# Kernel tuning notes

Hardware: AMD Instinct MI355X
Metric: run time of the kernel (lower is better)

Reference implementation:

```python
import jax, jax.numpy as jnp
import numpy as np

B, L, C = 4, 2052, 1024
H, D = 16, 64          # num_heads, head_dim
NREG = 4               # register tokens, bypass RoPE
LN_EPS = 1e-5


def setup_inputs() -> dict:
    key = jax.random.key(0)
    ks = jax.random.split(key, 6)
    s = 1.0 / np.sqrt(C)
    return {
        "x": jax.random.normal(ks[0], (B, L, C), jnp.float32),
        "rope_embed": jax.random.normal(ks[1], (2, L - NREG, D), jnp.float32),  # [cos; sin]
        "Wqkv": jax.random.normal(ks[2], (C, 3 * C), jnp.float32) * s,
        "bqkv": jnp.zeros((3 * C,), jnp.float32),
        "Wproj": jax.random.normal(ks[3], (C, C), jnp.float32) * s,
        "bproj": jnp.zeros((C,), jnp.float32),
        "ln_gamma": jnp.ones((C,), jnp.float32),
        "ln_beta": jnp.zeros((C,), jnp.float32),
    }


def _rotate_half(x):
    x1, x2 = jnp.split(x, 2, axis=-1)
    return jnp.concatenate([-x2, x1], axis=-1)


def _apply_rope(q, k, rope_embed, n_reg):
    # q,k: (B,H,L,D); rope_embed: (2, L-n_reg, D)
    cos = rope_embed[0][None, None]  # (1,1,Ls,D)
    sin = rope_embed[1][None, None]
    def rot(t):
        reg, sp = t[:, :, :n_reg], t[:, :, n_reg:]
        sp = sp * cos + _rotate_half(sp) * sin
        return jnp.concatenate([reg, sp], axis=2)
    return rot(q), rot(k)


def reference(x, rope_embed, Wqkv, bqkv, Wproj, bproj, ln_gamma, ln_beta):
    # QKV projection: (B,L,3C) -> (3,B,H,L,D)
    qkv = (x @ Wqkv + bqkv).reshape(B, L, 3, H, D).transpose(2, 0, 3, 1, 4)
    q, k, v = qkv[0], qkv[1], qkv[2]
    q, k = _apply_rope(q, k, rope_embed, NREG)
    # SDPA (no dropout, not causal)
    scale = 1.0 / np.sqrt(D)
    logits = jnp.einsum("bhqd,bhkd->bhqk", q, k) * scale
    attn = jax.nn.softmax(logits, axis=-1)
    out = jnp.einsum("bhqk,bhkd->bhqd", attn, v)
    out = out.transpose(0, 2, 1, 3).reshape(B, L, C)
    # post-attention LayerNorm
    mu = jnp.mean(out, axis=-1, keepdims=True)
    var = jnp.mean(jnp.square(out - mu), axis=-1, keepdims=True)
    out = (out - mu) * jax.lax.rsqrt(var + LN_EPS) * ln_gamma + ln_beta
    # output projection
    return out @ Wproj + bproj
```

## Files before the change

kernel.cpp:

```cpp
#include <hip/hip_runtime.h>
#include <hip/hip_bf16.h>

#define B_ 4
#define L_ 2052
#define C_ 1024
#define H_ 16
#define D_ 64
#define NREG_ 4
#define M_ (B_*L_)
#define LP_ 2056
#define QSC 0.18033688f

typedef short bf16x8 __attribute__((ext_vector_type(8)));
typedef float f32x4 __attribute__((ext_vector_type(4)));
typedef __hip_bfloat16 bf16;

#define MFMA(a,b,c) __builtin_amdgcn_mfma_f32_16x16x32_bf16(a,b,c,0,0,0)

__device__ inline float b2f(bf16 v){ return __bfloat162float(v); }
__device__ inline bf16  f2b(float v){ return __float2bfloat16(v); }
__device__ inline bf16x8 as8(int4 v){ union{int4 i; bf16x8 b;} u; u.i=v; return u.b; }

__device__ inline void gl_lds16(const void* g, void* l){
    __builtin_amdgcn_global_load_lds(
        (const __attribute__((address_space(1))) void*)g,
        (__attribute__((address_space(3))) void*)l,
        16, 0, 0);
}

__global__ __launch_bounds__(256)
void cvt_split(const float* __restrict__ in, bf16* __restrict__ hi,
               bf16* __restrict__ lo, int n)
{
    int i = (blockIdx.x*256 + threadIdx.x)*4;
    if (i >= n) return;
    float4 v = *(const float4*)(in + i);
    int2 hraw, lraw;
    bf16* hp = (bf16*)&hraw;
    bf16* lp = (bf16*)&lraw;
    float vv[4] = {v.x, v.y, v.z, v.w};
    #pragma unroll
    for (int j=0;j<4;++j){
        bf16 h = f2b(vv[j]);
        hp[j] = h;
        lp[j] = f2b(vv[j] - b2f(h));
    }
    *(int2*)(hi + i) = hraw;
    *(int2*)(lo + i) = lraw;
}

__global__ __launch_bounds__(256)
void transpose_cvt(const float* __restrict__ in, bf16* __restrict__ out,
                   int R, int Cc)
{
    __shared__ bf16 t[32][33];
    int bx = blockIdx.x * 32;
    int by = blockIdx.y * 32;
    int tx = threadIdx.x;
    int ty = threadIdx.y;
    #pragma unroll
    for (int i=0;i<4;++i){
        int r = by + ty + i*8;
        int c = bx + tx;
        t[ty+i*8][tx] = f2b(in[(size_t)r*Cc + c]);
    }
    __syncthreads();
    #pragma unroll
    for (int i=0;i<4;++i){
        int r = bx + ty + i*8;
        int c = by + tx;
        out[(size_t)r*R + c] = t[tx][ty+i*8];
    }
}

template<typename OutT, bool SPLIT>
__global__ __launch_bounds__(256,2)
void gemm_wide(const bf16* __restrict__ A, const bf16* __restrict__ Alo,
               const bf16* __restrict__ Bt, const float* __restrict__ bias,
               OutT* __restrict__ C, int M, int N, int K)
{
    __shared__ bf16 As[128*32];
    __shared__ bf16 Als[SPLIT ? 128*32 : 8];
    __shared__ bf16 Bs[256*32];

    int tid  = threadIdx.x;
    int lane = tid & 63, wave = tid >> 6;
    int wm = (wave>>1)*64, wn = (wave&1)*128;
    int bm = blockIdx.y*128, bn = blockIdx.x*256;
    int lrow = lane & 15;
    int quad = lane >> 4;
    int sw8  = (quad ^ ((lrow>>2)&3)) * 8;

    f32x4 acc[4][8] = {};

    for (int k0 = 0; k0 < K; k0 += 32) {
        #pragma unroll
        for (int it=0; it<2; ++it) {
            int o  = (wave*2+it)*1024 + lane*16;
            int r  = o >> 6;
            int p  = (o >> 4) & 3;
            int ls = p ^ ((r>>2)&3);
            int ga = bm + r; if (ga >= M) ga = M-1;
            gl_lds16(A + (size_t)ga*K + k0 + ls*8, &As[(wave*2+it)*512]);
            if constexpr (SPLIT)
                gl_lds16(Alo + (size_t)ga*K + k0 + ls*8, &Als[(wave*2+it)*512]);
        }
        #pragma unroll
        for (int it=0; it<4; ++it) {
            int o  = (wave*4+it)*1024 + lane*16;
            int r  = o >> 6;
            int p  = (o >> 4) & 3;
            int ls = p ^ ((r>>2)&3);
            gl_lds16(Bt + (size_t)(bn + r)*K + k0 + ls*8, &Bs[(wave*4+it)*512]);
        }
        __syncthreads();

        bf16x8 b[8];
        #pragma unroll
        for (int i=0;i<8;++i)
            b[i] = *(const bf16x8*)(&Bs[(wn+i*16+lrow)*32 + sw8]);
        #pragma unroll
        for (int mi=0;mi<4;++mi){
            bf16x8 a = *(const bf16x8*)(&As[(wm+mi*16+lrow)*32 + sw8]);
            #pragma unroll
            for (int ni=0;ni<8;++ni)
                acc[mi][ni] = MFMA(a, b[ni], acc[mi][ni]);
            if constexpr (SPLIT) {
                bf16x8 al = *(const bf16x8*)(&Als[(wm+mi*16+lrow)*32 + sw8]);
                #pragma unroll
                for (int ni=0;ni<8;++ni)
                    acc[mi][ni] = MFMA(al, b[ni], acc[mi][ni]);
            }
        }
        __syncthreads();
    }

    #pragma unroll
    for (int ni=0;ni<8;++ni){
        int col = bn + wn + ni*16 + lrow;
        float bv = bias[col];
        #pragma unroll
        for (int mi=0;mi<4;++mi){
            int rowb = bm + wm + mi*16 + quad*4;
            #pragma unroll
            for (int r=0;r<4;++r){
                int row = rowb + r;
                if (row < M) {
                    float v = acc[mi][ni][r] + bv;
                    if constexpr (sizeof(OutT)==4) C[(size_t)row*N + col] = v;
                    else                           C[(size_t)row*N + col] = f2b(v);
                }
            }
        }
    }
}

__global__ __launch_bounds__(256)
void rope_kernel(bf16* __restrict__ qkv, const float* __restrict__ rope)
{
    int idx = blockIdx.x*256 + threadIdx.x;
    int d = idx & 31;
    int h = (idx >> 5) & 15;
    int m = idx >> 9;
    if (m >= M_) return;
    int l = m % L_;
    if (l < NREG_) return;
    const float* cp = rope + (size_t)(l - NREG_)*D_;
    const float* sp = rope + (size_t)(L_ - NREG_)*D_ + (size_t)(l - NREG_)*D_;
    float c0 = cp[d], c1 = cp[d+32], s0 = sp[d], s1 = sp[d+32];
    size_t base = (size_t)m*3072 + h*64;
    {
        float a = b2f(qkv[base + d]), b = b2f(qkv[base + d + 32]);
        qkv[base + d]      = f2b(a*c0 - b*s0);
        qkv[base + d + 32] = f2b(b*c1 + a*s1);
    }
    {
        size_t kb = base + 1024;
        float a = b2f(qkv[kb + d]), b = b2f(qkv[kb + d + 32]);
        qkv[kb + d]      = f2b(a*c0 - b*s0);
        qkv[kb + d + 32] = f2b(b*c1 + a*s1);
    }
}

__global__ __launch_bounds__(256)
void transpose_v(const bf16* __restrict__ qkv, bf16* __restrict__ Vt)
{
    __shared__ bf16 t[64*72];
    int bh = blockIdx.y, lt = blockIdx.x;
    int b = bh >> 4, h = bh & 15;
    int tid = threadIdx.x;
    #pragma unroll
    for (int it=0; it<2; ++it){
        int i = tid + it*256;
        int il = i >> 3, c = (i&7)*8;
        int l = lt*64 + il;
        int4 v = {0,0,0,0};
        if (l < L_) v = *(const int4*)(qkv + ((size_t)b*L_ + l)*3072 + 2048 + h*64 + c);
        *(int4*)(&t[il*72 + c]) = v;
    }
    __syncthreads();
    #pragma unroll
    for (int it=0; it<2; ++it){
        int i = tid + it*256;
        int d = i >> 3, ck = (i&7)*8;
        if (lt*64 + ck + 8 <= LP_){
            union { int4 q; bf16 e[8]; } u;
            #pragma unroll
            for (int j=0;j<8;++j) u.e[j] = t[(ck+j)*72 + d];
            *(int4*)(&Vt[((size_t)bh*64 + d)*LP_ + lt*64 + ck]) = u.q;
        }
    }
}

__global__ __launch_bounds__(256)
void attn_kernel(const bf16* __restrict__ qkv, const bf16* __restrict__ Vt,
                 float* __restrict__ out)
{
    __shared__ bf16 sQ[128*72];
    __shared__ bf16 sK[64*72];
    __shared__ bf16 sV[64*72];

    int tid = threadIdx.x, lane = tid & 63, wave = tid >> 6;
    int lrow = lane & 15, lk8 = (lane>>4)*8, quad = lane >> 4;
    int qt = blockIdx.x, bh = blockIdx.y;
    int b  = bh >> 4, h = bh & 15;
    size_t rowbase = (size_t)b * L_;
    int q0 = qt * 128;

    #pragma unroll
    for (int it=0; it<4; ++it){
        int i = tid + it*256;
        int r = i >> 3;
        int c = (i & 7) * 8;
        int lq = q0 + r;
        int4 v = {0,0,0,0};
        if (lq < L_) v = *(const int4*)(qkv + (rowbase + lq)*3072 + h*64 + c);
        *(int4*)(&sQ[r*72 + c]) = v;
    }
    __syncthreads();

    bf16x8 qf[2][2];
    #pragma unroll
    for (int qi=0;qi<2;++qi)
        #pragma unroll
        for (int s=0;s<2;++s)
            qf[qi][s] = *(const bf16x8*)(&sQ[(wave*32 + qi*16 + lrow)*72 + s*32 + lk8]);

    f32x4 o_[2][4] = {};
    f32x4 lsum[2] = {};

    bf16x8 onesf;
    #pragma unroll
    for (int j=0;j<8;++j) onesf[j] = (short)0x3F80;

    const int nkt = (L_ + 63) / 64;

    int4 kr[2], vr[2];
    {
        #pragma unroll
        for (int it=0; it<2; ++it){
            int i = tid + it*256;
            int r = i >> 3, c = (i & 7)*8;
            int pr = (r & 0x23) | ((r & 0x0C) << 1) | ((r & 0x10) >> 2);
            kr[it] = *(const int4*)(qkv + (rowbase + pr)*3072 + 1024 + h*64 + c);
            vr[it] = *(const int4*)(Vt + ((size_t)bh*64 + r)*LP_ + c);
        }
    }

    for (int kt = 0; kt < nkt; ++kt) {
        __syncthreads();
        #pragma unroll
        for (int it=0; it<2; ++it){
            int i = tid + it*256;
            int r = i >> 3, c = (i & 7)*8;
            *(int4*)(&sK[r*72 + c]) = kr[it];
            *(int4*)(&sV[r*72 + c]) = vr[it];
        }
        __syncthreads();
        if (kt+1 < nkt){
            #pragma unroll
            for (int it=0; it<2; ++it){
                int i = tid + it*256;
                int r = i >> 3, c = (i & 7)*8;
                int pr = (r & 0x23) | ((r & 0x0C) << 1) | ((r & 0x10) >> 2);
                int lk = (kt+1)*64 + pr;
                kr[it] = (lk < L_) ? *(const int4*)(qkv + (rowbase+lk)*3072 + 1024 + h*64 + c)
                                   : (int4){0,0,0,0};
                int vc = (kt+1)*64 + c;
                vr[it] = (vc + 8 <= LP_) ? *(const int4*)(Vt + ((size_t)bh*64 + r)*LP_ + vc)
                                         : (int4){0,0,0,0};
            }
        }

        bool full = (kt != 32);
        int4 pb[2][2];

        #pragma unroll
        for (int ki=0; ki<4; ++ki){
            bf16x8 kf0 = *(const bf16x8*)(&sK[(ki*16+lrow)*72 + lk8]);
            bf16x8 kf1 = *(const bf16x8*)(&sK[(ki*16+lrow)*72 + 32 + lk8]);
            #pragma unroll
            for (int qi=0; qi<2; ++qi){
                f32x4 t = {};
                t = MFMA(kf0, qf[qi][0], t);
                t = MFMA(kf1, qf[qi][1], t);
                float p[4];
                #pragma unroll
                for (int r=0;r<4;++r){
                    float e = __builtin_amdgcn_exp2f(t[r]*QSC);
                    int keyi = (ki>>1)*32 + quad*8 + (ki&1)*4 + r;
                    p[r] = (full || (2048 + keyi) < L_) ? e : 0.f;
                }
                union { int2 d2; __hip_bfloat162 h2[2]; } u;
                u.h2[0] = __float22bfloat162_rn({p[0], p[1]});
                u.h2[1] = __float22bfloat162_rn({p[2], p[3]});
                if ((ki & 1) == 0){ pb[qi][ki>>1].x = u.d2.x; pb[qi][ki>>1].y = u.d2.y; }
                else              { pb[qi][ki>>1].z = u.d2.x; pb[qi][ki>>1].w = u.d2.y; }
            }
        }

        #pragma unroll
        for (int ni=0; ni<4; ++ni){
            bf16x8 vf0 = *(const bf16x8*)(&sV[(ni*16+lrow)*72 + lk8]);
            bf16x8 vf1 = *(const bf16x8*)(&sV[(ni*16+lrow)*72 + 32 + lk8]);
            #pragma unroll
            for (int mi=0; mi<2; ++mi){
                f32x4 t = o_[mi][ni];
                t = MFMA(vf0, as8(pb[mi][0]), t);
                t = MFMA(vf1, as8(pb[mi][1]), t);
                o_[mi][ni] = t;
            }
        }
        #pragma unroll
        for (int mi=0; mi<2; ++mi){
            lsum[mi] = MFMA(onesf, as8(pb[mi][0]), lsum[mi]);
            lsum[mi] = MFMA(onesf, as8(pb[mi][1]), lsum[mi]);
        }
    }

    #pragma unroll
    for (int mi=0; mi<2; ++mi){
        float inv = 1.f / lsum[mi][0];
        int lq = q0 + wave*32 + mi*16 + lrow;
        if (lq < L_){
            size_t base = (rowbase + lq)*1024 + h*64;
            #pragma unroll
            for (int ni=0; ni<4; ++ni){
                f32x4 t = o_[mi][ni];
                float4 w = {t[0]*inv, t[1]*inv, t[2]*inv, t[3]*inv};
                *(float4*)(&out[base + ni*16 + quad*4]) = w;
            }
        }
    }
}

__global__ __launch_bounds__(256)
void ln_kernel(const float* __restrict__ in, const float* __restrict__ gamma,
               const float* __restrict__ beta, bf16* __restrict__ y)
{
    int row = blockIdx.x;
    int tid = threadIdx.x;
    int wave = tid >> 6, lane = tid & 63;
    float4 v4 = *(const float4*)(in + (size_t)row*1024 + tid*4);
    float v[4] = {v4.x, v4.y, v4.z, v4.w};
    float s = 0.f, q = 0.f;
    #pragma unroll
    for (int j=0;j<4;++j){ s += v[j]; q += v[j]*v[j]; }
    #pragma unroll
    for (int o=1;o<64;o<<=1){ s += __shfl_xor(s, o); q += __shfl_xor(q, o); }
    __shared__ float sh[8];
    if (lane == 0){ sh[wave] = s; sh[4+wave] = q; }
    __syncthreads();
    s = sh[0]+sh[1]+sh[2]+sh[3];
    q = sh[4]+sh[5]+sh[6]+sh[7];
    float mu  = s * (1.f/1024.f);
    float var = q * (1.f/1024.f) - mu*mu;
    float rstd = rsqrtf(var + 1e-5f);
    int2 raw;
    bf16* ob = (bf16*)&raw;
    #pragma unroll
    for (int j=0;j<4;++j){
        float g = gamma[tid*4+j], be = beta[tid*4+j];
        ob[j] = f2b((v[j]-mu)*rstd*g + be);
    }
    *(int2*)(y + (size_t)row*1024 + tid*4) = raw;
}

extern "C" void kernel_launch(void* const* d_in, const int* in_sizes, int n_in,
                              void* d_out, int out_size, void* d_ws, size_t ws_size,
                              hipStream_t stream)
{
    const float* x     = (const float*)d_in[0];
    const float* rope  = (const float*)d_in[1];
    const float* Wqkv  = (const float*)d_in[2];
    const float* bqkv  = (const float*)d_in[3];
    const float* Wproj = (const float*)d_in[4];
    const float* bproj = (const float*)d_in[5];
    const float* lng   = (const float*)d_in[6];
    const float* lnb   = (const float*)d_in[7];
    float* out = (float*)d_out;

    char* ws = (char*)d_ws;
    size_t off = 0;
    auto alloc = [&](size_t bytes)->char* {
        char* p = ws + off;
        off += (bytes + 255) & ~(size_t)255;
        return p;
    };
    bf16* xhi    = (bf16*)alloc((size_t)M_*C_*2);
    bf16* xlo    = (bf16*)alloc((size_t)M_*C_*2);
    bf16* WqkvT  = (bf16*)alloc((size_t)3*C_*C_*2);
    bf16* WprojT = (bf16*)alloc((size_t)C_*C_*2);
    bf16* qkv    = (bf16*)alloc((size_t)M_*3*C_*2);
    bf16* Vt     = (bf16*)alloc((size_t)B_*H_*D_*LP_*2);

    float* attnF = (float*)xhi;
    bf16*  y     = qkv;

    cvt_split<<<M_*C_/1024, 256, 0, stream>>>(x, xhi, xlo, M_*C_);
    transpose_cvt<<<dim3(3*C_/32, C_/32), dim3(32,8), 0, stream>>>(Wqkv, WqkvT, C_, 3*C_);
    transpose_cvt<<<dim3(C_/32, C_/32), dim3(32,8), 0, stream>>>(Wproj, WprojT, C_, C_);
    gemm_wide<bf16, true><<<dim3(3*C_/256, (M_+127)/128), 256, 0, stream>>>(
        xhi, xlo, WqkvT, bqkv, qkv, M_, 3*C_, C_);
    rope_kernel<<<(M_*H_*32)/256, 256, 0, stream>>>(qkv, rope);
    transpose_v<<<dim3((L_+63)/64, B_*H_), 256, 0, stream>>>(qkv, Vt);
    attn_kernel<<<dim3((L_+127)/128, B_*H_), 256, 0, stream>>>(qkv, Vt, attnF);
    ln_kernel<<<M_, 256, 0, stream>>>(attnF, lng, lnb, y);
    gemm_wide<float, false><<<dim3(C_/256, (M_+127)/128), 256, 0, stream>>>(
        y, nullptr, WprojT, bproj, out, M_, C_, C_);
}
```

Before: 434.6 us.

## Double-buffer GEMM LDS tiles and fold hi/lo split into K dimension

The GEMM now keeps two LDS buffers and issues the global-to-LDS loads for the next K tile while the current tile is computed, so memory latency can overlap with MFMA work. The hi/lo bf16 split of x is stored side by side as one 2048-wide A matrix, and the B matrix index wraps at KB, so the split becomes a longer K loop instead of a second inner MFMA pass. LDS use per block doubles, which may lower occupancy. The code relies on a single barrier per iteration to order the async LDS loads against the reads.

```diff
diff --git a/kernel.cpp b/kernel.cpp
--- a/kernel.cpp
+++ b/kernel.cpp
@@ -29,8 +29,7 @@
 }
 
 __global__ __launch_bounds__(256)
-void cvt_split(const float* __restrict__ in, bf16* __restrict__ hi,
-               bf16* __restrict__ lo, int n)
+void cvt_split(const float* __restrict__ in, bf16* __restrict__ a2, int n)
 {
     int i = (blockIdx.x*256 + threadIdx.x)*4;
     if (i >= n) return;
@@ -45,8 +44,10 @@
         hp[j] = h;
         lp[j] = f2b(vv[j] - b2f(h));
     }
-    *(int2*)(hi + i) = hraw;
-    *(int2*)(lo + i) = lraw;
+    int row = i >> 10, col = i & 1023;
+    size_t base = (size_t)row*2048 + col;
+    *(int2*)(a2 + base)        = hraw;
+    *(int2*)(a2 + base + 1024) = lraw;
 }
 
 __global__ __launch_bounds__(256)
@@ -73,15 +74,14 @@
     }
 }
 
-template<typename OutT, bool SPLIT>
+template<typename OutT>
 __global__ __launch_bounds__(256,2)
-void gemm_wide(const bf16* __restrict__ A, const bf16* __restrict__ Alo,
-               const bf16* __restrict__ Bt, const float* __restrict__ bias,
-               OutT* __restrict__ C, int M, int N, int K)
-{
-    __shared__ bf16 As[128*32];
-    __shared__ bf16 Als[SPLIT ? 128*32 : 8];
-    __shared__ bf16 Bs[256*32];
+void gemm_dbuf(const bf16* __restrict__ A, const bf16* __restrict__ Bt,
+               const float* __restrict__ bias, OutT* __restrict__ C,
+               int M, int N, int K, int KB)
+{
+    __shared__ bf16 As[2][128*32];
+    __shared__ bf16 Bs[2][256*32];
 
     int tid  = threadIdx.x;
     int lane = tid & 63, wave = tid >> 6;
@@ -93,7 +93,8 @@
 
     f32x4 acc[4][8] = {};
 
-    for (int k0 = 0; k0 < K; k0 += 32) {
+    auto STAGE = [&](int buf, int k0){
+        int kb = (k0 >= KB) ? k0 - KB : k0;
         #pragma unroll
         for (int it=0; it<2; ++it) {
             int o  = (wave*2+it)*1024 + lane*16;
@@ -101,9 +102,7 @@
             int p  = (o >> 4) & 3;
             int ls = p ^ ((r>>2)&3);
             int ga = bm + r; if (ga >= M) ga = M-1;
-            gl_lds16(A + (size_t)ga*K + k0 + ls*8, &As[(wave*2+it)*512]);
-            if constexpr (SPLIT)
-                gl_lds16(Alo + (size_t)ga*K + k0 + ls*8, &Als[(wave*2+it)*512]);
+            gl_lds16(A + (size_t)ga*K + k0 + ls*8, &As[buf][(wave*2+it)*512]);
         }
         #pragma unroll
         for (int it=0; it<4; ++it) {
@@ -111,28 +110,31 @@
             int r  = o >> 6;
             int p  = (o >> 4) & 3;
             int ls = p ^ ((r>>2)&3);
-            gl_lds16(Bt + (size_t)(bn + r)*K + k0 + ls*8, &Bs[(wave*4+it)*512]);
-        }
-        __syncthreads();
+            gl_lds16(Bt + (size_t)(bn + r)*KB + kb + ls*8, &Bs[buf][(wave*4+it)*512]);
+        }
+    };
+
+    int nt = K >> 5;
+    int cur = 0;
+    STAGE(0, 0);
+    __syncthreads();
+
+    for (int t = 0; t < nt; ++t) {
+        if (t+1 < nt) STAGE(cur^1, (t+1)*32);
 
         bf16x8 b[8];
         #pragma unroll
         for (int i=0;i<8;++i)
-            b[i] = *(const bf16x8*)(&Bs[(wn+i*16+lrow)*32 + sw8]);
+            b[i] = *(const bf16x8*)(&Bs[cur][(wn+i*16+lrow)*32 + sw8]);
         #pragma unroll
         for (int mi=0;mi<4;++mi){
-            bf16x8 a = *(const bf16x8*)(&As[(wm+mi*16+lrow)*32 + sw8]);
+            bf16x8 a = *(const bf16x8*)(&As[cur][(wm+mi*16+lrow)*32 + sw8]);
             #pragma unroll
             for (int ni=0;ni<8;++ni)
                 acc[mi][ni] = MFMA(a, b[ni], acc[mi][ni]);
-            if constexpr (SPLIT) {
-                bf16x8 al = *(const bf16x8*)(&Als[(wm+mi*16+lrow)*32 + sw8]);
-                #pragma unroll
-                for (int ni=0;ni<8;++ni)
-                    acc[mi][ni] = MFMA(al, b[ni], acc[mi][ni]);
-            }
         }
         __syncthreads();
+        cur ^= 1;
     }
 
     #pragma unroll
@@ -407,25 +409,24 @@
         off += (bytes + 255) & ~(size_t)255;
         return p;
     };
-    bf16* xhi    = (bf16*)alloc((size_t)M_*C_*2);
-    bf16* xlo    = (bf16*)alloc((size_t)M_*C_*2);
+    bf16* A2     = (bf16*)alloc((size_t)M_*2048*2);
     bf16* WqkvT  = (bf16*)alloc((size_t)3*C_*C_*2);
     bf16* WprojT = (bf16*)alloc((size_t)C_*C_*2);
     bf16* qkv    = (bf16*)alloc((size_t)M_*3*C_*2);
     bf16* Vt     = (bf16*)alloc((size_t)B_*H_*D_*LP_*2);
 
-    float* attnF = (float*)xhi;
+    float* attnF = (float*)A2;
     bf16*  y     = qkv;
 
-    cvt_split<<<M_*C_/1024, 256, 0, stream>>>(x, xhi, xlo, M_*C_);
+    cvt_split<<<M_*C_/1024, 256, 0, stream>>>(x, A2, M_*C_);
     transpose_cvt<<<dim3(3*C_/32, C_/32), dim3(32,8), 0, stream>>>(Wqkv, WqkvT, C_, 3*C_);
     transpose_cvt<<<dim3(C_/32, C_/32), dim3(32,8), 0, stream>>>(Wproj, WprojT, C_, C_);
-    gemm_wide<bf16, true><<<dim3(3*C_/256, (M_+127)/128), 256, 0, stream>>>(
-        xhi, xlo, WqkvT, bqkv, qkv, M_, 3*C_, C_);
+    gemm_dbuf<bf16><<<dim3(3*C_/256, (M_+127)/128), 256, 0, stream>>>(
+        A2, WqkvT, bqkv, qkv, M_, 3*C_, 2048, C_);
     rope_kernel<<<(M_*H_*32)/256, 256, 0, stream>>>(qkv, rope);
     transpose_v<<<dim3((L_+63)/64, B_*H_), 256, 0, stream>>>(qkv, Vt);
     attn_kernel<<<dim3((L_+127)/128, B_*H_), 256, 0, stream>>>(qkv, Vt, attnF);
     ln_kernel<<<M_, 256, 0, stream>>>(attnF, lng, lnb, y);
-    gemm_wide<float, false><<<dim3(C_/256, (M_+127)/128), 256, 0, stream>>>(
-        y, nullptr, WprojT, bproj, out, M_, C_, C_);
-}
+    gemm_dbuf<float><<<dim3(C_/256, (M_+127)/128), 256, 0, stream>>>(
+        y, WprojT, bproj, out, M_, C_, C_, C_);
+}
```

New measurement: 475.0 us. +9.3%, slower.

## Load K/V MFMA fragments directly from global memory, dropping LDS staging

Applied to the files above, without the earlier changes.

The attention kernel no longer stages K and V tiles through shared memory with register prefetch and two barriers per tile. Each lane instead loads its MFMA fragments straight from global (L2-cached) memory, and the final partial key tile is peeled out of the loop so the masking check leaves the main loop. This removes the LDS round-trip and the per-tile synchronisation. In exchange, every wave re-reads K/V from global memory, with more redundant traffic and latency exposed, since there is no explicit prefetch.

```diff
diff --git a/kernel.cpp b/kernel.cpp
--- a/kernel.cpp
+++ b/kernel.cpp
@@ -217,8 +217,6 @@
                  float* __restrict__ out)
 {
     __shared__ bf16 sQ[128*72];
-    __shared__ bf16 sK[64*72];
-    __shared__ bf16 sV[64*72];
 
     int tid = threadIdx.x, lane = tid & 63, wave = tid >> 6;
     int lrow = lane & 15, lk8 = (lane>>4)*8, quad = lane >> 4;
@@ -253,52 +251,73 @@
     #pragma unroll
     for (int j=0;j<8;++j) onesf[j] = (short)0x3F80;
 
-    const int nkt = (L_ + 63) / 64;
-
-    int4 kr[2], vr[2];
+    int pk[4];
+    #pragma unroll
+    for (int ki=0;ki<4;++ki){
+        int s = ki*16 + lrow;
+        pk[ki] = (s & 0x23) | ((s & 0x0C) << 1) | ((s & 0x10) >> 2);
+    }
+
+    const bf16* kbase = qkv + rowbase*3072 + 1024 + h*64 + lk8;
+    const bf16* vbase = Vt + (size_t)bh*64*LP_ + lk8;
+
+    for (int kt = 0; kt < 32; ++kt) {
+        int4 pb[2][2];
+
+        const bf16* kb = kbase + (size_t)kt*64*3072;
+        #pragma unroll
+        for (int ki=0; ki<4; ++ki){
+            const bf16* kp = kb + (size_t)pk[ki]*3072;
+            bf16x8 kf0 = *(const bf16x8*)(kp);
+            bf16x8 kf1 = *(const bf16x8*)(kp + 32);
+            #pragma unroll
+            for (int qi=0; qi<2; ++qi){
+                f32x4 t = {};
+                t = MFMA(kf0, qf[qi][0], t);
+                t = MFMA(kf1, qf[qi][1], t);
+                float p[4];
+                #pragma unroll
+                for (int r=0;r<4;++r)
+                    p[r] = __builtin_amdgcn_exp2f(t[r]*QSC);
+                union { int2 d2; __hip_bfloat162 h2[2]; } u;
+                u.h2[0] = __float22bfloat162_rn({p[0], p[1]});
+                u.h2[1] = __float22bfloat162_rn({p[2], p[3]});
+                if ((ki & 1) == 0){ pb[qi][ki>>1].x = u.d2.x; pb[qi][ki>>1].y = u.d2.y; }
+                else              { pb[qi][ki>>1].z = u.d2.x; pb[qi][ki>>1].w = u.d2.y; }
+            }
+        }
+
+        const bf16* vb = vbase + kt*64;
+        #pragma unroll
+        for (int ni=0; ni<4; ++ni){
+            const bf16* vp = vb + (size_t)(ni*16+lrow)*LP_;
+            bf16x8 vf0 = *(const bf16x8*)(vp);
+            bf16x8 vf1 = *(const bf16x8*)(vp + 32);
+            #pragma unroll
+            for (int mi=0; mi<2; ++mi){
+                f32x4 t = o_[mi][ni];
+                t = MFMA(vf0, as8(pb[mi][0]), t);
+                t = MFMA(vf1, as8(pb[mi][1]), t);
+                o_[mi][ni] = t;
+            }
+        }
+        #pragma unroll
+        for (int mi=0; mi<2; ++mi){
+            lsum[mi] = MFMA(onesf, as8(pb[mi][0]), lsum[mi]);
+            lsum[mi] = MFMA(onesf, as8(pb[mi][1]), lsum[mi]);
+        }
+    }
+
     {
-        #pragma unroll
-        for (int it=0; it<2; ++it){
-            int i = tid + it*256;
-            int r = i >> 3, c = (i & 7)*8;
-            int pr = (r & 0x23) | ((r & 0x0C) << 1) | ((r & 0x10) >> 2);
-            kr[it] = *(const int4*)(qkv + (rowbase + pr)*3072 + 1024 + h*64 + c);
-            vr[it] = *(const int4*)(Vt + ((size_t)bh*64 + r)*LP_ + c);
-        }
-    }
-
-    for (int kt = 0; kt < nkt; ++kt) {
-        __syncthreads();
-        #pragma unroll
-        for (int it=0; it<2; ++it){
-            int i = tid + it*256;
-            int r = i >> 3, c = (i & 7)*8;
-            *(int4*)(&sK[r*72 + c]) = kr[it];
-            *(int4*)(&sV[r*72 + c]) = vr[it];
-        }
-        __syncthreads();
-        if (kt+1 < nkt){
-            #pragma unroll
-            for (int it=0; it<2; ++it){
-                int i = tid + it*256;
-                int r = i >> 3, c = (i & 7)*8;
-                int pr = (r & 0x23) | ((r & 0x0C) << 1) | ((r & 0x10) >> 2);
-                int lk = (kt+1)*64 + pr;
-                kr[it] = (lk < L_) ? *(const int4*)(qkv + (rowbase+lk)*3072 + 1024 + h*64 + c)
-                                   : (int4){0,0,0,0};
-                int vc = (kt+1)*64 + c;
-                vr[it] = (vc + 8 <= LP_) ? *(const int4*)(Vt + ((size_t)bh*64 + r)*LP_ + vc)
-                                         : (int4){0,0,0,0};
-            }
-        }
-
-        bool full = (kt != 32);
         int4 pb[2][2];
-
+        const bf16* kb = kbase + (size_t)2048*3072;
         #pragma unroll
         for (int ki=0; ki<4; ++ki){
-            bf16x8 kf0 = *(const bf16x8*)(&sK[(ki*16+lrow)*72 + lk8]);
-            bf16x8 kf1 = *(const bf16x8*)(&sK[(ki*16+lrow)*72 + 32 + lk8]);
+            int row = 2048 + pk[ki];
+            const bf16* kp = (row < L_) ? (kb + (size_t)pk[ki]*3072)
+                                        : (kbase);
+            bf16x8 kf0 = *(const bf16x8*)(kp);
+            bf16x8 kf1 = *(const bf16x8*)(kp + 32);
             #pragma unroll
             for (int qi=0; qi<2; ++qi){
                 f32x4 t = {};
@@ -309,7 +328,7 @@
                 for (int r=0;r<4;++r){
                     float e = __builtin_amdgcn_exp2f(t[r]*QSC);
                     int keyi = (ki>>1)*32 + quad*8 + (ki&1)*4 + r;
-                    p[r] = (full || (2048 + keyi) < L_) ? e : 0.f;
+                    p[r] = (2048 + keyi < L_) ? e : 0.f;
                 }
                 union { int2 d2; __hip_bfloat162 h2[2]; } u;
                 u.h2[0] = __float22bfloat162_rn({p[0], p[1]});
@@ -319,10 +338,13 @@
             }
         }
 
+        const bf16* vb = vbase + 2048;
         #pragma unroll
         for (int ni=0; ni<4; ++ni){
-            bf16x8 vf0 = *(const bf16x8*)(&sV[(ni*16+lrow)*72 + lk8]);
-            bf16x8 vf1 = *(const bf16x8*)(&sV[(ni*16+lrow)*72 + 32 + lk8]);
+            bf16x8 vf0 = {};
+            bf16x8 vf1 = {};
+            if (lk8 == 0)
+                vf0 = *(const bf16x8*)(vb + (size_t)(ni*16+lrow)*LP_);
             #pragma unroll
             for (int mi=0; mi<2; ++mi){
                 f32x4 t = o_[mi][ni];
```

After: 583.6 us. 34.3% more time.

## Load attention tiles via direct global-to-LDS with XOR swizzle, larger Q tile

Applied to the files above, without the earlier changes.

The attention kernel now stages Q, K and V tiles with global_load_lds directly into shared memory using an XOR-swizzled 64-wide layout instead of padded 72-wide rows. This drops the register-staged prefetch. Each block now covers 192 query rows (48 per wave), up from 128, to reuse K/V more, and launch bounds request 2 blocks per CU. The cost is that loads are no longer overlapped with compute (load, sync, compute, sync), register pressure rises from the bigger accumulators, and the grid shrinks.

```diff
diff --git a/kernel.cpp b/kernel.cpp
--- a/kernel.cpp
+++ b/kernel.cpp
@@ -212,95 +212,83 @@
     }
 }
 
-__global__ __launch_bounds__(256)
+__global__ __launch_bounds__(256,2)
 void attn_kernel(const bf16* __restrict__ qkv, const bf16* __restrict__ Vt,
                  float* __restrict__ out)
 {
-    __shared__ bf16 sQ[128*72];
-    __shared__ bf16 sK[64*72];
-    __shared__ bf16 sV[64*72];
+    __shared__ bf16 sQ[192*64];
+    __shared__ bf16 sK[64*64];
+    __shared__ bf16 sV[64*64];
 
     int tid = threadIdx.x, lane = tid & 63, wave = tid >> 6;
-    int lrow = lane & 15, lk8 = (lane>>4)*8, quad = lane >> 4;
+    int lrow = lane & 15, quad = lane >> 4;
     int qt = blockIdx.x, bh = blockIdx.y;
     int b  = bh >> 4, h = bh & 15;
     size_t rowbase = (size_t)b * L_;
-    int q0 = qt * 128;
-
-    #pragma unroll
-    for (int it=0; it<4; ++it){
-        int i = tid + it*256;
-        int r = i >> 3;
-        int c = (i & 7) * 8;
-        int lq = q0 + r;
-        int4 v = {0,0,0,0};
-        if (lq < L_) v = *(const int4*)(qkv + (rowbase + lq)*3072 + h*64 + c);
-        *(int4*)(&sQ[r*72 + c]) = v;
+    int q0 = qt * 192;
+
+    int l8   = lane >> 3;
+    int p3   = lane & 7;
+    int swz0 = (quad     ^ (lrow&7))*8;
+    int swz1 = ((4+quad) ^ (lrow&7))*8;
+
+    #pragma unroll
+    for (int it=0; it<6; ++it){
+        int ci  = wave*6 + it;
+        int row = ci*8 + l8;
+        int ls  = p3 ^ (row&7);
+        int gq  = q0 + row; if (gq >= L_) gq = L_-1;
+        gl_lds16(qkv + (rowbase + gq)*3072 + h*64 + ls*8, &sQ[ci*512]);
     }
     __syncthreads();
 
-    bf16x8 qf[2][2];
-    #pragma unroll
-    for (int qi=0;qi<2;++qi)
-        #pragma unroll
-        for (int s=0;s<2;++s)
-            qf[qi][s] = *(const bf16x8*)(&sQ[(wave*32 + qi*16 + lrow)*72 + s*32 + lk8]);
-
-    f32x4 o_[2][4] = {};
-    f32x4 lsum[2] = {};
+    bf16x8 qf[3][2];
+    #pragma unroll
+    for (int qi=0;qi<3;++qi){
+        qf[qi][0] = *(const bf16x8*)(&sQ[(wave*48 + qi*16 + lrow)*64 + swz0]);
+        qf[qi][1] = *(const bf16x8*)(&sQ[(wave*48 + qi*16 + lrow)*64 + swz1]);
+    }
+
+    f32x4 o_[3][4] = {};
+    f32x4 lsum[3] = {};
 
     bf16x8 onesf;
     #pragma unroll
     for (int j=0;j<8;++j) onesf[j] = (short)0x3F80;
 
-    const int nkt = (L_ + 63) / 64;
-
-    int4 kr[2], vr[2];
-    {
+    const bf16* kgbase = qkv + rowbase*3072 + 1024 + h*64;
+    const bf16* vgbase = Vt + (size_t)bh*64*LP_;
+
+    for (int kt = 0; kt <= 32; ++kt) {
         #pragma unroll
         for (int it=0; it<2; ++it){
-            int i = tid + it*256;
-            int r = i >> 3, c = (i & 7)*8;
-            int pr = (r & 0x23) | ((r & 0x0C) << 1) | ((r & 0x10) >> 2);
-            kr[it] = *(const int4*)(qkv + (rowbase + pr)*3072 + 1024 + h*64 + c);
-            vr[it] = *(const int4*)(Vt + ((size_t)bh*64 + r)*LP_ + c);
-        }
-    }
-
-    for (int kt = 0; kt < nkt; ++kt) {
+            int ci  = wave*2 + it;
+            int row = ci*8 + l8;
+            int ls  = p3 ^ (row&7);
+            int key = kt*64 + ((row & 0x23) | ((row & 0x0C) << 1) | ((row & 0x10) >> 2));
+            if (key >= L_) key = L_-1;
+            gl_lds16(kgbase + (size_t)key*3072 + ls*8, &sK[ci*512]);
+        }
+        #pragma unroll
+        for (int it=0; it<2; ++it){
+            int ci  = wave*2 + it;
+            int row = ci*8 + l8;
+            int ls  = p3 ^ (row&7);
+            int col = kt*64 + ls*8;
+            if (col + 8 > LP_) col = 0;
+            gl_lds16(vgbase + (size_t)row*LP_ + col, &sV[ci*512]);
+        }
         __syncthreads();
-        #pragma unroll
-        for (int it=0; it<2; ++it){
-            int i = tid + it*256;
-            int r = i >> 3, c = (i & 7)*8;
-            *(int4*)(&sK[r*72 + c]) = kr[it];
-            *(int4*)(&sV[r*72 + c]) = vr[it];
-        }
-        __syncthreads();
-        if (kt+1 < nkt){
-            #pragma unroll
-            for (int it=0; it<2; ++it){
-                int i = tid + it*256;
-                int r = i >> 3, c = (i & 7)*8;
-                int pr = (r & 0x23) | ((r & 0x0C) << 1) | ((r & 0x10) >> 2);
-                int lk = (kt+1)*64 + pr;
-                kr[it] = (lk < L_) ? *(const int4*)(qkv + (rowbase+lk)*3072 + 1024 + h*64 + c)
-                                   : (int4){0,0,0,0};
-                int vc = (kt+1)*64 + c;
-                vr[it] = (vc + 8 <= LP_) ? *(const int4*)(Vt + ((size_t)bh*64 + r)*LP_ + vc)
-                                         : (int4){0,0,0,0};
-            }
-        }
 
         bool full = (kt != 32);
-        int4 pb[2][2];
+        int4 pb[3][2];
 
         #pragma unroll
         for (int ki=0; ki<4; ++ki){
-            bf16x8 kf0 = *(const bf16x8*)(&sK[(ki*16+lrow)*72 + lk8]);
-            bf16x8 kf1 = *(const bf16x8*)(&sK[(ki*16+lrow)*72 + 32 + lk8]);
-            #pragma unroll
-            for (int qi=0; qi<2; ++qi){
+            bf16x8 kf0 = *(const bf16x8*)(&sK[(ki*16+lrow)*64 + swz0]);
+            bf16x8 kf1 = *(const bf16x8*)(&sK[(ki*16+lrow)*64 + swz1]);
+            #pragma unroll
+            for (int qi=0; qi<3; ++qi){
                 f32x4 t = {};
                 t = MFMA(kf0, qf[qi][0], t);
                 t = MFMA(kf1, qf[qi][1], t);
@@ -321,10 +309,10 @@
 
         #pragma unroll
         for (int ni=0; ni<4; ++ni){
-            bf16x8 vf0 = *(const bf16x8*)(&sV[(ni*16+lrow)*72 + lk8]);
-            bf16x8 vf1 = *(const bf16x8*)(&sV[(ni*16+lrow)*72 + 32 + lk8]);
-            #pragma unroll
-            for (int mi=0; mi<2; ++mi){
+            bf16x8 vf0 = *(const bf16x8*)(&sV[(ni*16+lrow)*64 + swz0]);
+            bf16x8 vf1 = *(const bf16x8*)(&sV[(ni*16+lrow)*64 + swz1]);
+            #pragma unroll
+            for (int mi=0; mi<3; ++mi){
                 f32x4 t = o_[mi][ni];
                 t = MFMA(vf0, as8(pb[mi][0]), t);
                 t = MFMA(vf1, as8(pb[mi][1]), t);
@@ -332,16 +320,17 @@
             }
         }
         #pragma unroll
-        for (int mi=0; mi<2; ++mi){
+        for (int mi=0; mi<3; ++mi){
             lsum[mi] = MFMA(onesf, as8(pb[mi][0]), lsum[mi]);
             lsum[mi] = MFMA(onesf, as8(pb[mi][1]), lsum[mi]);
         }
-    }
-
-    #pragma unroll
-    for (int mi=0; mi<2; ++mi){
+        __syncthreads();
+    }
+
+    #pragma unroll
+    for (int mi=0; mi<3; ++mi){
         float inv = 1.f / lsum[mi][0];
-        int lq = q0 + wave*32 + mi*16 + lrow;
+        int lq = q0 + wave*48 + mi*16 + lrow;
         if (lq < L_){
             size_t base = (rowbase + lq)*1024 + h*64;
             #pragma unroll
@@ -424,7 +413,7 @@
         xhi, xlo, WqkvT, bqkv, qkv, M_, 3*C_, C_);
     rope_kernel<<<(M_*H_*32)/256, 256, 0, stream>>>(qkv, rope);
     transpose_v<<<dim3((L_+63)/64, B_*H_), 256, 0, stream>>>(qkv, Vt);
-    attn_kernel<<<dim3((L_+127)/128, B_*H_), 256, 0, stream>>>(qkv, Vt, attnF);
+    attn_kernel<<<dim3((L_+191)/192, B_*H_), 256, 0, stream>>>(qkv, Vt, attnF);
     ln_kernel<<<M_, 256, 0, stream>>>(attnF, lng, lnb, y);
     gemm_wide<float, false><<<dim3(C_/256, (M_+127)/128), 256, 0, stream>>>(
         y, nullptr, WprojT, bproj, out, M_, C_, C_);
```

After: 420.5 us. 1.03x faster.
